# Kernel tuning notes

Measured on AMD Instinct MI355X. Metric: run time of the kernel, lower is better.

## Reference

```python
import jax, jax.numpy as jnp
import numpy as np

E = 2048
H = 16
D = E // H  # head_dim = 128


def setup_inputs() -> dict:
    key = jax.random.key(0)
    ks = jax.random.split(key, 8)
    s = 0.02
    x = jax.random.normal(ks[0], (2, 2048, E), dtype=jnp.float32)
    Wq = jax.random.normal(ks[1], (E, E), dtype=jnp.float32) * s
    Wk = jax.random.normal(ks[2], (E, E), dtype=jnp.float32) * s
    Wv = jax.random.normal(ks[3], (E, E), dtype=jnp.float32) * s
    W1 = jax.random.normal(ks[4], (2 * E, E), dtype=jnp.float32) * s
    b1 = jax.random.normal(ks[5], (2 * E,), dtype=jnp.float32) * s
    W2 = jax.random.normal(ks[6], (E, 2 * E), dtype=jnp.float32) * s
    b2 = jax.random.normal(ks[7], (E,), dtype=jnp.float32) * s
    return {"x": x, "Wq": Wq, "Wk": Wk, "Wv": Wv, "W1": W1, "b1": b1, "W2": W2, "b2": b2}


def reference(x, Wq, Wk, Wv, W1, b1, W2, b2):
    B, S, _ = x.shape
    # QKV projections (torch Linear: x @ W.T), reshape to (B,S,H,D)
    q = (x @ Wq.T).reshape(B, S, H, D)
    k = (x @ Wk.T).reshape(B, S, H, D)
    v = (x @ Wv.T).reshape(B, S, H, D)
    # scores: (B,H,S,S)
    score = jnp.einsum('bqhd,bkhd->bhqk', q, k)
    # causal mask added BEFORE scaling (as in original; -inf unaffected by scale)
    causal = jnp.tril(jnp.ones((S, S), dtype=bool))
    score = jnp.where(causal, score, -jnp.inf)
    score = score / jnp.sqrt(jnp.float32(D))
    attn = jax.nn.softmax(score, axis=-1)
    o = jnp.einsum('bhqk,bkhd->bqhd', attn, v).reshape(B, S, E)
    # FFN with hidden = 2*E, no residual connections in this block
    h = jax.nn.gelu(o @ W1.T + b1)
    return h @ W2.T + b2
```

## Files before the change

### kernel.cpp

```cpp
#include <hip/hip_runtime.h>
#include <cmath>


typedef _Float16 half8 __attribute__((ext_vector_type(8)));
typedef _Float16 half4v __attribute__((ext_vector_type(4)));
typedef float float4v __attribute__((ext_vector_type(4)));

__device__ inline void load_lds16(const _Float16* g, _Float16* l) {
  __builtin_amdgcn_global_load_lds(
      (const __attribute__((address_space(1))) void*)g,
      (__attribute__((address_space(3))) void*)l, 16, 0, 0);
}

__global__ void cvt_kernel(const float* __restrict__ s0, const float* __restrict__ s1,
                           const float* __restrict__ s2, const float* __restrict__ s3,
                           _Float16* d0, _Float16* d1, _Float16* d2, _Float16* d3,
                           int n0, int n1, int n2, int n3, float sc1) {
  const float* s;
  _Float16* d;
  int n;
  float sc = 1.0f;
  switch (blockIdx.y) {
    case 0: s = s0; d = d0; n = n0; break;
    case 1: s = s1; d = d1; n = n1; sc = sc1; break;
    case 2: s = s2; d = d2; n = n2; break;
    default: s = s3; d = d3; n = n3; break;
  }
  const int step = gridDim.x * 256 * 4;
  for (int i = (blockIdx.x * 256 + threadIdx.x) * 4; i < n; i += step) {
    float4v v = *(const float4v*)&s[i];
    half4v h;
#pragma unroll
    for (int e = 0; e < 4; e++) h[e] = (_Float16)(v[e] * sc);
    *(half4v*)&d[i] = h;
  }
}

__device__ __forceinline__ void gemm8_core(
    const _Float16* __restrict__ A, const _Float16* __restrict__ B, int Kloop,
    int Kstride, int bm, int bn, _Float16* lds, float4v acc[8][4]) {
  const int tid = threadIdx.x;
  const int w = tid >> 6, lane = tid & 63;
  const int l16 = lane & 15, quad = lane >> 4;
  const int srow = w * 16 + (lane >> 2);
  const int clocal = ((lane & 3) * 8) ^ ((lane & 32) ? 16 : 0);
  int rdh = (l16 << 5) + (quad << 3);
  rdh ^= (l16 & 8) << 1;

  const _Float16* pA0 = A + (size_t)(bm + srow) * Kstride + clocal;
  const _Float16* pA1 = A + (size_t)(bm + 128 + srow) * Kstride + clocal;
  const _Float16* pB0 = B + (size_t)(bn + srow) * Kstride + clocal;
  const _Float16* pB1 = B + (size_t)(bn + 128 + srow) * Kstride + clocal;

  _Float16* const dA0 = lds + w * 1024;
  _Float16* const dA1 = lds + 8192 + w * 1024;
  _Float16* const dB0 = lds + 16384 + w * 1024;
  _Float16* const dB1 = lds + 24576 + w * 1024;

  const int aH = w >> 2, bH = (w >> 1) & 1, bRB = (w & 1) * 4;
  const _Float16* const rA0 = lds + aH * 8192;
  const _Float16* const rB0 = lds + 16384 + bH * 8192;
  const _Float16* const rA1 = rA0 + 32768;
  const _Float16* const rB1 = rB0 + 32768;

  const int NT = Kloop >> 6;

#define STG(p, d, kt)                     \
  do {                                    \
    const _Float16* _s = (p) + (kt) * 64; \
    load_lds16(_s, (d));                  \
    load_lds16(_s + 32, (d) + 512);       \
  } while (0)
#define BARRIER() asm volatile("s_barrier" ::: "memory")
#define WAIT_LGKM()                                  \
  asm volatile("s_waitcnt lgkmcnt(0)" ::: "memory"); \
  __builtin_amdgcn_sched_barrier(0);
#define RD_A(base, RB0)                                                       \
  _Pragma("unroll") for (int rb = 0; rb < 4; rb++)                            \
  _Pragma("unroll") for (int ks = 0; ks < 2; ks++)                            \
      af[rb][ks] = *(const half8*)&(base)[((((RB0) + rb) * 2 + ks) << 9) + rdh];
#define RD_B(base, J0)                                                        \
  _Pragma("unroll") for (int j = 0; j < 2; j++)                               \
  _Pragma("unroll") for (int ks = 0; ks < 2; ks++)                            \
      bf[(J0) + j][ks] =                                                      \
          *(const half8*)&(base)[(((bRB + (J0) + j) * 2 + ks) << 9) + rdh];
#define MFMA_Q(RB0, J0)                                                       \
  __builtin_amdgcn_s_setprio(1);                                              \
  _Pragma("unroll") for (int rb = 0; rb < 4; rb++)                            \
  _Pragma("unroll") for (int j = 0; j < 2; j++)                               \
  _Pragma("unroll") for (int ks = 0; ks < 2; ks++)                            \
      acc[(RB0) + rb][(J0) + j] = __builtin_amdgcn_mfma_f32_16x16x32_f16(     \
          af[rb][ks], bf[(J0) + j][ks], acc[(RB0) + rb][(J0) + j], 0, 0, 0);  \
  __builtin_amdgcn_s_setprio(0);                                              \
  BARRIER();

  STG(pB0, dB0, 0); STG(pB1, dB1, 0); STG(pA0, dA0, 0); STG(pA1, dA1, 0);
  STG(pB0, dB0 + 32768, 1); STG(pB1, dB1 + 32768, 1);
  asm volatile("s_waitcnt vmcnt(4)" ::: "memory");
  BARRIER();

  half8 af[4][2], bf[4][2];

  for (int t = 0; t < NT; t += 2) {
    const bool last = (t + 2 >= NT);
    RD_A(rA0, 0) RD_B(rB0, 0)
    STG(pA0, dA0 + 32768, t + 1);
    BARRIER(); WAIT_LGKM()
    MFMA_Q(0, 0)
    RD_B(rB0, 2)
    STG(pA1, dA1 + 32768, t + 1);
    BARRIER(); WAIT_LGKM()
    MFMA_Q(0, 2)
    RD_A(rA0, 4)
    if (!last) STG(pB0, dB0, t + 2);
    BARRIER(); WAIT_LGKM()
    MFMA_Q(4, 0)
    if (!last) {
      STG(pA0, dA0, t + 2);
      asm volatile("s_waitcnt vmcnt(4)" ::: "memory");
    } else {
      asm volatile("s_waitcnt vmcnt(0)" ::: "memory");
    }
    BARRIER();
    MFMA_Q(4, 2)
    RD_A(rA1, 0) RD_B(rB1, 0)
    if (!last) STG(pA1, dA1, t + 2);
    BARRIER(); WAIT_LGKM()
    MFMA_Q(0, 0)
    RD_B(rB1, 2)
    if (!last) STG(pB1, dB1, t + 2);
    BARRIER(); WAIT_LGKM()
    MFMA_Q(0, 2)
    RD_A(rA1, 4)
    if (!last) STG(pB0, dB0 + 32768, t + 3);
    BARRIER(); WAIT_LGKM()
    MFMA_Q(4, 0)
    if (!last) {
      STG(pB1, dB1 + 32768, t + 3);
      asm volatile("s_waitcnt vmcnt(4)" ::: "memory");
    }
    BARRIER();
    MFMA_Q(4, 2)
  }
#undef STG
#undef BARRIER
#undef WAIT_LGKM
#undef RD_A
#undef RD_B
#undef MFMA_Q
}

__global__ __launch_bounds__(512, 2) void gemm_qkv(
    const _Float16* __restrict__ xh, const _Float16* __restrict__ Wq,
    const _Float16* __restrict__ Wk, const _Float16* __restrict__ Wv,
    _Float16* __restrict__ Qh, _Float16* __restrict__ Kh,
    _Float16* __restrict__ Vt) {
  __shared__ __align__(16) _Float16 lds[67584];
  const int z = blockIdx.z;
  const _Float16* B = (z == 0) ? Wq : (z == 1 ? Wk : Wv);
  const int bm = blockIdx.y * 256, bn = blockIdx.x * 256;
  float4v acc[8][4] = {};
  gemm8_core(xh, B, 2048, 2048, bm, bn, lds, acc);

  const int tid = threadIdx.x;
  const int w = tid >> 6, lane = tid & 63;
  const int l16 = lane & 15, quad = lane >> 4;
  const int wm = (w >> 2) * 128, wn = (w & 3) * 64;
  if (z == 2) {
    _Float16* Tr = lds;
    __syncthreads();
#pragma unroll
    for (int j = 0; j < 4; j++) {
      const int cl = wn + j * 16 + l16;
#pragma unroll
      for (int rb = 0; rb < 8; rb++) {
        const int ml = wm + rb * 16 + quad * 4;
#pragma unroll
        for (int reg = 0; reg < 4; reg++)
          Tr[cl * 264 + ml + reg] = (_Float16)acc[rb][j][reg];
      }
    }
    __syncthreads();
    const int cl = tid >> 1;
    const int ml = (tid & 1) * 128;
    const int mg = bm + ml;
    _Float16* dst = Vt + ((size_t)(mg >> 11) << 22) +
                    ((size_t)(bn + cl) << 11) + (mg & 2047);
#pragma unroll
    for (int i = 0; i < 16; i++)
      *(half8*)(dst + i * 8) = *(const half8*)&Tr[cl * 264 + ml + i * 8];
  } else {
    _Float16* outRM = z ? Kh : Qh;
#pragma unroll
    for (int j = 0; j < 4; j++) {
      const int col = bn + wn + j * 16 + l16;
#pragma unroll
      for (int rb = 0; rb < 8; rb++) {
        const int rbase = bm + wm + rb * 16 + quad * 4;
#pragma unroll
        for (int reg = 0; reg < 4; reg++)
          outRM[(size_t)(rbase + reg) * 2048 + col] = (_Float16)acc[rb][j][reg];
      }
    }
  }
}

__global__ __launch_bounds__(512, 2) void gemm_ffn1(
    const _Float16* __restrict__ A, const _Float16* __restrict__ B,
    const float* __restrict__ bias, _Float16* __restrict__ out, int N, int K) {
  __shared__ __align__(16) _Float16 lds[65536];
  const int bm = blockIdx.y * 256, bn = blockIdx.x * 256;
  float4v acc[8][4] = {};
  gemm8_core(A, B, K, K, bm, bn, lds, acc);

  const int tid = threadIdx.x;
  const int w = tid >> 6, lane = tid & 63;
  const int l16 = lane & 15, quad = lane >> 4;
  const int wm = (w >> 2) * 128, wn = (w & 3) * 64;
#pragma unroll
  for (int j = 0; j < 4; j++) {
    const int col = bn + wn + j * 16 + l16;
    const float bv = bias[col];
#pragma unroll
    for (int rb = 0; rb < 8; rb++) {
      const int rbase = bm + wm + rb * 16 + quad * 4;
#pragma unroll
      for (int reg = 0; reg < 4; reg++) {
        const int m = rbase + reg;
        const float x = acc[rb][j][reg] + bv;
        const float inner = 0.7978845608028654f * (x + 0.044715f * x * x * x);
        out[(size_t)m * N + col] = (_Float16)(0.5f * x * (1.0f + tanhf(inner)));
      }
    }
  }
}

__global__ __launch_bounds__(512, 2) void gemm_ffn2_part(
    const _Float16* __restrict__ A, const _Float16* __restrict__ B,
    float* __restrict__ p0, float* __restrict__ p1) {
  __shared__ __align__(16) _Float16 lds[65536];
  const int bm = blockIdx.y * 256, bn = blockIdx.x * 256;
  const int k0 = blockIdx.z * 2048;
  float* out = blockIdx.z ? p1 : p0;
  float4v acc[8][4] = {};
  gemm8_core(A + k0, B + k0, 2048, 4096, bm, bn, lds, acc);

  const int tid = threadIdx.x;
  const int w = tid >> 6, lane = tid & 63;
  const int l16 = lane & 15, quad = lane >> 4;
  const int wm = (w >> 2) * 128, wn = (w & 3) * 64;
#pragma unroll
  for (int j = 0; j < 4; j++) {
    const int col = bn + wn + j * 16 + l16;
#pragma unroll
    for (int rb = 0; rb < 8; rb++) {
      const int rbase = bm + wm + rb * 16 + quad * 4;
#pragma unroll
      for (int reg = 0; reg < 4; reg++)
        out[(size_t)(rbase + reg) * 2048 + col] = acc[rb][j][reg];
    }
  }
}

__global__ void reduce_add(float* __restrict__ out, const float* __restrict__ p0,
                           const float* __restrict__ b2, int n) {
  const int step = gridDim.x * 256 * 4;
  for (int i = (blockIdx.x * 256 + threadIdx.x) * 4; i < n; i += step) {
    float4v a = *(const float4v*)&out[i];
    float4v b = *(const float4v*)&p0[i];
    float4v bb = *(const float4v*)&b2[i & 2047];
    float4v r;
#pragma unroll
    for (int e = 0; e < 4; e++) r[e] = a[e] + b[e] + bb[e];
    *(float4v*)&out[i] = r;
  }
}

__global__ __launch_bounds__(256, 2) void attn_mfma(
    const _Float16* __restrict__ Qh, const _Float16* __restrict__ Kh,
    const _Float16* __restrict__ Vt, _Float16* __restrict__ Oh) {
  __shared__ __align__(16) _Float16 Ksh[64][136];
  __shared__ __align__(16) _Float16 Vsh[128][72];
  __shared__ __align__(16) _Float16 Psh[4][32][72];

  const int b = blockIdx.z;
  int qt = blockIdx.x;
  if (b) qt = gridDim.x - 1 - qt;
  const int h = blockIdx.y;
  const int tid = threadIdx.x;
  const int wave = tid >> 6, lane = tid & 63;
  const int l16 = lane & 15, quad = lane >> 4;
  const int q0 = qt * 128;
  const int wq0 = q0 + wave * 32;

  half8 qf[2][4];
#pragma unroll
  for (int rb = 0; rb < 2; rb++)
#pragma unroll
    for (int kc = 0; kc < 4; kc++)
      qf[rb][kc] = *(const half8*)(Qh +
          (size_t)(b * 2048 + wq0 + rb * 16 + l16) * 2048 + h * 128 +
          kc * 32 + quad * 8);

  half8 ones;
#pragma unroll
  for (int e = 0; e < 8; e++) ones[e] = (_Float16)1.0f;

  const int kkey = tid >> 2, kd = (tid & 3) * 32;
  const int vd = tid >> 1, vkey = (tid & 1) * 32;

  half8 kpre[4], vpre[4];
  {
    const _Float16* p = Kh + (size_t)(b * 2048 + kkey) * 2048 + h * 128 + kd;
#pragma unroll
    for (int i = 0; i < 4; i++) kpre[i] = *(const half8*)(p + i * 8);
    const _Float16* pv = Vt + ((size_t)b << 22) + (size_t)(h * 128 + vd) * 2048 + vkey;
#pragma unroll
    for (int i = 0; i < 4; i++) vpre[i] = *(const half8*)(pv + i * 8);
  }

  float4v o[2][9] = {};
  float4v mrow[2];
#pragma unroll
  for (int rb = 0; rb < 2; rb++)
#pragma unroll
    for (int e = 0; e < 4; e++) mrow[rb][e] = -INFINITY;

  const int nkb = qt * 2 + 2;
  for (int kb = 0; kb < nkb; kb++) {
    const int k0 = kb * 64;
    __syncthreads();
#pragma unroll
    for (int i = 0; i < 4; i++) *(half8*)&Ksh[kkey][kd + i * 8] = kpre[i];
#pragma unroll
    for (int i = 0; i < 4; i++) *(half8*)&Vsh[vd][vkey + i * 8] = vpre[i];
    __syncthreads();

    if (kb + 1 < nkb) {
      const int k1 = k0 + 64;
      const _Float16* p = Kh + (size_t)(b * 2048 + k1 + kkey) * 2048 + h * 128 + kd;
#pragma unroll
      for (int i = 0; i < 4; i++) kpre[i] = *(const half8*)(p + i * 8);
      const _Float16* pv = Vt + ((size_t)b << 22) + (size_t)(h * 128 + vd) * 2048 + k1 + vkey;
#pragma unroll
      for (int i = 0; i < 4; i++) vpre[i] = *(const half8*)(pv + i * 8);
    }

    if (k0 <= wq0 + 31) {
      float4v s[2][4] = {};
#pragma unroll
      for (int kc = 0; kc < 4; kc++) {
#pragma unroll
        for (int cb = 0; cb < 4; cb++) {
          half8 kf = *(const half8*)&Ksh[cb * 16 + l16][kc * 32 + quad * 8];
#pragma unroll
          for (int rb = 0; rb < 2; rb++)
            s[rb][cb] = __builtin_amdgcn_mfma_f32_16x16x32_f16(qf[rb][kc], kf, s[rb][cb], 0, 0, 0);
        }
      }
      if (k0 + 63 > wq0) {
#pragma unroll
        for (int cb = 0; cb < 4; cb++)
#pragma unroll
          for (int rb = 0; rb < 2; rb++)
#pragma unroll
            for (int reg = 0; reg < 4; reg++) {
              const int key = k0 + cb * 16 + l16;
              const int row = wq0 + rb * 16 + quad * 4 + reg;
              if (key > row) s[rb][cb][reg] = -INFINITY;
            }
      }
#pragma unroll
      for (int rb = 0; rb < 2; rb++) {
        float4v mt;
#pragma unroll
        for (int e = 0; e < 4; e++)
          mt[e] = fmaxf(fmaxf(s[rb][0][e], s[rb][1][e]),
                        fmaxf(s[rb][2][e], s[rb][3][e]));
#pragma unroll
        for (int msk = 1; msk <= 8; msk <<= 1)
#pragma unroll
          for (int e = 0; e < 4; e++) mt[e] = fmaxf(mt[e], __shfl_xor(mt[e], msk, 64));
        int need = 0;
#pragma unroll
        for (int e = 0; e < 4; e++) need |= (mt[e] > mrow[rb][e] + 8.0f) ? 1 : 0;
        if (__any(need)) {
          float4v al;
#pragma unroll
          for (int e = 0; e < 4; e++) {
            const float mn = fmaxf(mrow[rb][e], mt[e]);
            al[e] = exp2f(mrow[rb][e] - mn);
            mrow[rb][e] = mn;
          }
#pragma unroll
          for (int cd = 0; cd < 9; cd++)
#pragma unroll
            for (int e = 0; e < 4; e++) o[rb][cd][e] *= al[e];
        }
#pragma unroll
        for (int cb = 0; cb < 4; cb++) {
#pragma unroll
          for (int e = 0; e < 4; e++) s[rb][cb][e] = exp2f(s[rb][cb][e] - mrow[rb][e]);
#pragma unroll
          for (int e = 0; e < 4; e++)
            Psh[wave][rb * 16 + quad * 4 + e][cb * 16 + l16] = (_Float16)s[rb][cb][e];
        }
      }
      half8 pf[2][2];
#pragma unroll
      for (int rb = 0; rb < 2; rb++)
#pragma unroll
        for (int kc = 0; kc < 2; kc++)
          pf[rb][kc] = *(const half8*)&Psh[wave][rb * 16 + l16][kc * 32 + quad * 8];
#pragma unroll
      for (int cd = 0; cd < 8; cd++) {
#pragma unroll
        for (int kc = 0; kc < 2; kc++) {
          half8 vf = *(const half8*)&Vsh[cd * 16 + l16][kc * 32 + quad * 8];
#pragma unroll
          for (int rb = 0; rb < 2; rb++)
            o[rb][cd] = __builtin_amdgcn_mfma_f32_16x16x32_f16(pf[rb][kc], vf, o[rb][cd], 0, 0, 0);
        }
      }
#pragma unroll
      for (int kc = 0; kc < 2; kc++)
#pragma unroll
        for (int rb = 0; rb < 2; rb++)
          o[rb][8] = __builtin_amdgcn_mfma_f32_16x16x32_f16(pf[rb][kc], ones, o[rb][8], 0, 0, 0);
    }
  }

#pragma unroll
  for (int rb = 0; rb < 2; rb++) {
    float4v inv;
#pragma unroll
    for (int e = 0; e < 4; e++) inv[e] = 1.0f / o[rb][8][e];
#pragma unroll
    for (int cd = 0; cd < 8; cd++)
#pragma unroll
      for (int reg = 0; reg < 4; reg++)
        Oh[(size_t)(b * 2048 + wq0 + rb * 16 + quad * 4 + reg) * 2048 +
           h * 128 + cd * 16 + l16] = (_Float16)(o[rb][cd][reg] * inv[reg]);
  }
}

extern "C" void kernel_launch(void* const* d_in, const int* in_sizes, int n_in,
                              void* d_out, int out_size, void* d_ws,
                              size_t ws_size, hipStream_t stream) {
  const float* x = (const float*)d_in[0];
  const float* Wq = (const float*)d_in[1];
  const float* Wk = (const float*)d_in[2];
  const float* Wv = (const float*)d_in[3];
  const float* W1 = (const float*)d_in[4];
  const float* b1 = (const float*)d_in[5];
  const float* W2 = (const float*)d_in[6];
  const float* b2 = (const float*)d_in[7];
  float* out = (float*)d_out;

  const int ME = 8388608;
  const int EE = 4194304;

  _Float16* ws = (_Float16*)d_ws;
  _Float16* xh  = ws;
  _Float16* Wqh = xh + ME;
  _Float16* Wkh = Wqh + EE;
  _Float16* Wvh = Wkh + EE;
  _Float16* Qh  = Wvh + EE;
  _Float16* Kh  = Qh + ME;
  _Float16* Vt  = Kh + ME;
  _Float16* Oh  = xh;
  _Float16* W1h = Wqh;
  _Float16* W2h = Vt;
  _Float16* Hid = Qh;
  float*    P0  = (float*)ws;

  const float qscale = 1.4426950408889634f * 0.08838834764831845f;

  cvt_kernel<<<dim3(1024, 4), 256, 0, stream>>>(x, Wq, Wk, Wv, xh, Wqh, Wkh, Wvh,
                                                ME, EE, EE, EE, qscale);
  gemm_qkv<<<dim3(8, 16, 3), 512, 0, stream>>>(xh, Wqh, Wkh, Wvh, Qh, Kh, Vt);
  attn_mfma<<<dim3(16, 16, 2), 256, 0, stream>>>(Qh, Kh, Vt, Oh);
  cvt_kernel<<<dim3(1024, 2), 256, 0, stream>>>(W1, W2, nullptr, nullptr,
                                                W1h, W2h, nullptr, nullptr,
                                                ME, ME, 0, 0, 1.0f);
  gemm_ffn1<<<dim3(16, 16), 512, 0, stream>>>(Oh, W1h, b1, Hid, 4096, 2048);
  gemm_ffn2_part<<<dim3(8, 16, 2), 512, 0, stream>>>(Hid, W2h, P0, out);
  reduce_add<<<dim3(2048), 256, 0, stream>>>(out, P0, b2, ME);
}
```

Before: 546.9 us.

## Stage GEMM and attention epilogues through LDS for vectorized row-major stores

Replaces scattered 2-byte per-element global stores in the QKV, FFN1 and attention output epilogues with a two-pass transpose through XOR-swizzled shared memory, followed by coalesced 16-byte stores. FFN1's tanh-GELU is rewritten as x*sigmoid(2*inner) using exp2f, which is cheaper than tanhf. In attention, the cross-lane max shuffle now runs only when a rescale is actually needed, skipping that reduction on most tiles. The extra barriers and LDS round trips in the epilogues are the cost.

```diff
diff --git a/kernel.cpp b/kernel.cpp
--- a/kernel.cpp
+++ b/kernel.cpp
@@ -150,6 +150,29 @@
 #undef MFMA_Q
 }
 
+#define EPILOGUE_RM(outp, N, VALEXPR)                                         \
+  {                                                                           \
+    _Float16(*Tr)[264] = (_Float16(*)[264])lds;                               \
+    _Pragma("unroll 1") for (int hp = 0; hp < 2; hp++) {                      \
+      __syncthreads();                                                        \
+      if ((w >> 2) == hp) {                                                   \
+        _Pragma("unroll") for (int j = 0; j < 4; j++)                         \
+        _Pragma("unroll") for (int rb = 0; rb < 8; rb++)                      \
+        _Pragma("unroll") for (int reg = 0; reg < 4; reg++) {                 \
+          const int rr = rb * 16 + quad * 4 + reg;                            \
+          Tr[rr][(wn + j * 16 + l16) ^ ((rr & 7) << 3)] =                     \
+              (_Float16)(VALEXPR);                                            \
+        }                                                                     \
+      }                                                                       \
+      __syncthreads();                                                        \
+      const int r = tid >> 2, cc = (tid & 3) * 64;                            \
+      const int xr = (r & 7) << 3;                                            \
+      _Float16* dst = (outp) + (size_t)(bm + hp * 128 + r) * (N) + bn + cc;   \
+      _Pragma("unroll") for (int i = 0; i < 8; i++)                           \
+          *(half8*)(dst + i * 8) = *(const half8*)&Tr[r][(cc + i * 8) ^ xr];  \
+    }                                                                         \
+  }
+
 __global__ __launch_bounds__(512, 2) void gemm_qkv(
     const _Float16* __restrict__ xh, const _Float16* __restrict__ Wq,
     const _Float16* __restrict__ Wk, const _Float16* __restrict__ Wv,
@@ -191,17 +214,7 @@
       *(half8*)(dst + i * 8) = *(const half8*)&Tr[cl * 264 + ml + i * 8];
   } else {
     _Float16* outRM = z ? Kh : Qh;
-#pragma unroll
-    for (int j = 0; j < 4; j++) {
-      const int col = bn + wn + j * 16 + l16;
-#pragma unroll
-      for (int rb = 0; rb < 8; rb++) {
-        const int rbase = bm + wm + rb * 16 + quad * 4;
-#pragma unroll
-        for (int reg = 0; reg < 4; reg++)
-          outRM[(size_t)(rbase + reg) * 2048 + col] = (_Float16)acc[rb][j][reg];
-      }
-    }
+    EPILOGUE_RM(outRM, 2048, acc[rb][j][reg])
   }
 }
 
@@ -216,23 +229,21 @@
   const int tid = threadIdx.x;
   const int w = tid >> 6, lane = tid & 63;
   const int l16 = lane & 15, quad = lane >> 4;
-  const int wm = (w >> 2) * 128, wn = (w & 3) * 64;
+  const int wn = (w & 3) * 64;
 #pragma unroll
   for (int j = 0; j < 4; j++) {
-    const int col = bn + wn + j * 16 + l16;
-    const float bv = bias[col];
-#pragma unroll
-    for (int rb = 0; rb < 8; rb++) {
-      const int rbase = bm + wm + rb * 16 + quad * 4;
+    const float bv = bias[bn + wn + j * 16 + l16];
+#pragma unroll
+    for (int rb = 0; rb < 8; rb++)
 #pragma unroll
       for (int reg = 0; reg < 4; reg++) {
-        const int m = rbase + reg;
         const float x = acc[rb][j][reg] + bv;
-        const float inner = 0.7978845608028654f * (x + 0.044715f * x * x * x);
-        out[(size_t)m * N + col] = (_Float16)(0.5f * x * (1.0f + tanhf(inner)));
+        const float t = x + 0.044715f * x * x * x;
+        const float e = exp2f(-2.302208198f * t);
+        acc[rb][j][reg] = x / (1.0f + e);
       }
-    }
-  }
+  }
+  EPILOGUE_RM(out, N, acc[rb][j][reg])
 }
 
 __global__ __launch_bounds__(512, 2) void gemm_ffn2_part(
@@ -377,14 +388,14 @@
         for (int e = 0; e < 4; e++)
           mt[e] = fmaxf(fmaxf(s[rb][0][e], s[rb][1][e]),
                         fmaxf(s[rb][2][e], s[rb][3][e]));
-#pragma unroll
-        for (int msk = 1; msk <= 8; msk <<= 1)
-#pragma unroll
-          for (int e = 0; e < 4; e++) mt[e] = fmaxf(mt[e], __shfl_xor(mt[e], msk, 64));
         int need = 0;
 #pragma unroll
         for (int e = 0; e < 4; e++) need |= (mt[e] > mrow[rb][e] + 8.0f) ? 1 : 0;
         if (__any(need)) {
+#pragma unroll
+          for (int msk = 1; msk <= 8; msk <<= 1)
+#pragma unroll
+            for (int e = 0; e < 4; e++) mt[e] = fmaxf(mt[e], __shfl_xor(mt[e], msk, 64));
           float4v al;
 #pragma unroll
           for (int e = 0; e < 4; e++) {
@@ -430,17 +441,32 @@
     }
   }
 
-#pragma unroll
-  for (int rb = 0; rb < 2; rb++) {
-    float4v inv;
-#pragma unroll
-    for (int e = 0; e < 4; e++) inv[e] = 1.0f / o[rb][8][e];
-#pragma unroll
-    for (int cd = 0; cd < 8; cd++)
-#pragma unroll
-      for (int reg = 0; reg < 4; reg++)
-        Oh[(size_t)(b * 2048 + wq0 + rb * 16 + quad * 4 + reg) * 2048 +
-           h * 128 + cd * 16 + l16] = (_Float16)(o[rb][cd][reg] * inv[reg]);
+  float4v inv[2];
+#pragma unroll
+  for (int rb = 0; rb < 2; rb++)
+#pragma unroll
+    for (int e = 0; e < 4; e++) inv[rb][e] = 1.0f / o[rb][8][e];
+
+#pragma unroll 1
+  for (int p = 0; p < 2; p++) {
+    __syncthreads();
+    if ((wave >> 1) == p) {
+      _Float16* slab = &Ksh[(wave & 1) * 32][0];
+#pragma unroll
+      for (int rb = 0; rb < 2; rb++)
+#pragma unroll
+        for (int cd = 0; cd < 8; cd++)
+#pragma unroll
+          for (int reg = 0; reg < 4; reg++)
+            slab[(rb * 16 + quad * 4 + reg) * 136 + cd * 16 + l16] =
+                (_Float16)(o[rb][cd][reg] * inv[rb][reg]);
+    }
+    __syncthreads();
+    const int r = tid >> 2, c = (tid & 3) * 8;
+    _Float16* dst = Oh + (size_t)(b * 2048 + q0 + p * 64 + r) * 2048 + h * 128 + c;
+#pragma unroll
+    for (int i = 0; i < 4; i++)
+      *(half8*)(dst + i * 32) = *(const half8*)&Ksh[r][c + i * 32];
   }
 }
 
```

Result: slower. 566.5 us (+3.6%).

## Enlarge attention tiles to 256 queries and 128-key blocks, stage output via LDS

Applied to the files above, without the earlier changes.

The attention kernel moves to 512-thread blocks, each covering 256 query rows, and processes 128 keys per iteration. This halves the number of K/V tile loads and barriers per query row. The cross-lane max reduction now runs only when a rescale is needed, and the output is staged through LDS so global writes are coalesced 16-byte stores. GELU in FFN1 is rewritten from tanh to an equivalent exp2-based sigmoid form. In exchange the kernel uses much more LDS, which limits it to one block per CU, and it drops the reversed-tile ordering that balanced causal work across batches.

```diff
diff --git a/kernel.cpp b/kernel.cpp
--- a/kernel.cpp
+++ b/kernel.cpp
@@ -228,8 +228,9 @@
       for (int reg = 0; reg < 4; reg++) {
         const int m = rbase + reg;
         const float x = acc[rb][j][reg] + bv;
-        const float inner = 0.7978845608028654f * (x + 0.044715f * x * x * x);
-        out[(size_t)m * N + col] = (_Float16)(0.5f * x * (1.0f + tanhf(inner)));
+        const float t = x + 0.044715f * x * x * x;
+        const float e = exp2f(-2.302208198f * t);
+        out[(size_t)m * N + col] = (_Float16)(x / (1.0f + e));
       }
     }
   }
@@ -276,21 +277,20 @@
   }
 }
 
-__global__ __launch_bounds__(256, 2) void attn_mfma(
+__global__ __launch_bounds__(512, 2) void attn_mfma(
     const _Float16* __restrict__ Qh, const _Float16* __restrict__ Kh,
     const _Float16* __restrict__ Vt, _Float16* __restrict__ Oh) {
-  __shared__ __align__(16) _Float16 Ksh[64][136];
-  __shared__ __align__(16) _Float16 Vsh[128][72];
-  __shared__ __align__(16) _Float16 Psh[4][32][72];
+  __shared__ __align__(16) _Float16 Ksh[128][136];
+  __shared__ __align__(16) _Float16 Vsh[128][136];
+  __shared__ __align__(16) _Float16 Psh[8][32][136];
 
   const int b = blockIdx.z;
-  int qt = blockIdx.x;
-  if (b) qt = gridDim.x - 1 - qt;
+  const int qt = blockIdx.x;
   const int h = blockIdx.y;
   const int tid = threadIdx.x;
   const int wave = tid >> 6, lane = tid & 63;
   const int l16 = lane & 15, quad = lane >> 4;
-  const int q0 = qt * 128;
+  const int q0 = qt * 256;
   const int wq0 = q0 + wave * 32;
 
   half8 qf[2][4];
@@ -307,7 +307,7 @@
   for (int e = 0; e < 8; e++) ones[e] = (_Float16)1.0f;
 
   const int kkey = tid >> 2, kd = (tid & 3) * 32;
-  const int vd = tid >> 1, vkey = (tid & 1) * 32;
+  const int vd = tid >> 2, vkey = (tid & 3) * 32;
 
   half8 kpre[4], vpre[4];
   {
@@ -328,7 +328,7 @@
 
   const int nkb = qt * 2 + 2;
   for (int kb = 0; kb < nkb; kb++) {
-    const int k0 = kb * 64;
+    const int k0 = kb * 128;
     __syncthreads();
 #pragma unroll
     for (int i = 0; i < 4; i++) *(half8*)&Ksh[kkey][kd + i * 8] = kpre[i];
@@ -337,7 +337,7 @@
     __syncthreads();
 
     if (kb + 1 < nkb) {
-      const int k1 = k0 + 64;
+      const int k1 = k0 + 128;
       const _Float16* p = Kh + (size_t)(b * 2048 + k1 + kkey) * 2048 + h * 128 + kd;
 #pragma unroll
       for (int i = 0; i < 4; i++) kpre[i] = *(const half8*)(p + i * 8);
@@ -347,20 +347,20 @@
     }
 
     if (k0 <= wq0 + 31) {
-      float4v s[2][4] = {};
+      float4v s[2][8] = {};
 #pragma unroll
       for (int kc = 0; kc < 4; kc++) {
 #pragma unroll
-        for (int cb = 0; cb < 4; cb++) {
+        for (int cb = 0; cb < 8; cb++) {
           half8 kf = *(const half8*)&Ksh[cb * 16 + l16][kc * 32 + quad * 8];
 #pragma unroll
           for (int rb = 0; rb < 2; rb++)
             s[rb][cb] = __builtin_amdgcn_mfma_f32_16x16x32_f16(qf[rb][kc], kf, s[rb][cb], 0, 0, 0);
         }
       }
-      if (k0 + 63 > wq0) {
-#pragma unroll
-        for (int cb = 0; cb < 4; cb++)
+      if (k0 + 127 > wq0) {
+#pragma unroll
+        for (int cb = 0; cb < 8; cb++)
 #pragma unroll
           for (int rb = 0; rb < 2; rb++)
 #pragma unroll
@@ -374,17 +374,21 @@
       for (int rb = 0; rb < 2; rb++) {
         float4v mt;
 #pragma unroll
-        for (int e = 0; e < 4; e++)
-          mt[e] = fmaxf(fmaxf(s[rb][0][e], s[rb][1][e]),
-                        fmaxf(s[rb][2][e], s[rb][3][e]));
-#pragma unroll
-        for (int msk = 1; msk <= 8; msk <<= 1)
-#pragma unroll
-          for (int e = 0; e < 4; e++) mt[e] = fmaxf(mt[e], __shfl_xor(mt[e], msk, 64));
+        for (int e = 0; e < 4; e++) {
+          float m01 = fmaxf(s[rb][0][e], s[rb][1][e]);
+          float m23 = fmaxf(s[rb][2][e], s[rb][3][e]);
+          float m45 = fmaxf(s[rb][4][e], s[rb][5][e]);
+          float m67 = fmaxf(s[rb][6][e], s[rb][7][e]);
+          mt[e] = fmaxf(fmaxf(m01, m23), fmaxf(m45, m67));
+        }
         int need = 0;
 #pragma unroll
         for (int e = 0; e < 4; e++) need |= (mt[e] > mrow[rb][e] + 8.0f) ? 1 : 0;
         if (__any(need)) {
+#pragma unroll
+          for (int msk = 1; msk <= 8; msk <<= 1)
+#pragma unroll
+            for (int e = 0; e < 4; e++) mt[e] = fmaxf(mt[e], __shfl_xor(mt[e], msk, 64));
           float4v al;
 #pragma unroll
           for (int e = 0; e < 4; e++) {
@@ -398,7 +402,7 @@
             for (int e = 0; e < 4; e++) o[rb][cd][e] *= al[e];
         }
 #pragma unroll
-        for (int cb = 0; cb < 4; cb++) {
+        for (int cb = 0; cb < 8; cb++) {
 #pragma unroll
           for (int e = 0; e < 4; e++) s[rb][cb][e] = exp2f(s[rb][cb][e] - mrow[rb][e]);
 #pragma unroll
@@ -406,16 +410,16 @@
             Psh[wave][rb * 16 + quad * 4 + e][cb * 16 + l16] = (_Float16)s[rb][cb][e];
         }
       }
-      half8 pf[2][2];
+      half8 pf[2][4];
 #pragma unroll
       for (int rb = 0; rb < 2; rb++)
 #pragma unroll
-        for (int kc = 0; kc < 2; kc++)
+        for (int kc = 0; kc < 4; kc++)
           pf[rb][kc] = *(const half8*)&Psh[wave][rb * 16 + l16][kc * 32 + quad * 8];
 #pragma unroll
       for (int cd = 0; cd < 8; cd++) {
 #pragma unroll
-        for (int kc = 0; kc < 2; kc++) {
+        for (int kc = 0; kc < 4; kc++) {
           half8 vf = *(const half8*)&Vsh[cd * 16 + l16][kc * 32 + quad * 8];
 #pragma unroll
           for (int rb = 0; rb < 2; rb++)
@@ -423,24 +427,39 @@
         }
       }
 #pragma unroll
-      for (int kc = 0; kc < 2; kc++)
+      for (int kc = 0; kc < 4; kc++)
 #pragma unroll
         for (int rb = 0; rb < 2; rb++)
           o[rb][8] = __builtin_amdgcn_mfma_f32_16x16x32_f16(pf[rb][kc], ones, o[rb][8], 0, 0, 0);
     }
   }
 
-#pragma unroll
-  for (int rb = 0; rb < 2; rb++) {
-    float4v inv;
-#pragma unroll
-    for (int e = 0; e < 4; e++) inv[e] = 1.0f / o[rb][8][e];
-#pragma unroll
-    for (int cd = 0; cd < 8; cd++)
-#pragma unroll
-      for (int reg = 0; reg < 4; reg++)
-        Oh[(size_t)(b * 2048 + wq0 + rb * 16 + quad * 4 + reg) * 2048 +
-           h * 128 + cd * 16 + l16] = (_Float16)(o[rb][cd][reg] * inv[reg]);
+  float4v inv[2];
+#pragma unroll
+  for (int rb = 0; rb < 2; rb++)
+#pragma unroll
+    for (int e = 0; e < 4; e++) inv[rb][e] = 1.0f / o[rb][8][e];
+
+#pragma unroll 1
+  for (int p = 0; p < 2; p++) {
+    __syncthreads();
+    if ((wave >> 2) == p) {
+      _Float16* slab = &Ksh[(wave & 3) * 32][0];
+#pragma unroll
+      for (int rb = 0; rb < 2; rb++)
+#pragma unroll
+        for (int cd = 0; cd < 8; cd++)
+#pragma unroll
+          for (int reg = 0; reg < 4; reg++)
+            slab[(rb * 16 + quad * 4 + reg) * 136 + cd * 16 + l16] =
+                (_Float16)(o[rb][cd][reg] * inv[rb][reg]);
+    }
+    __syncthreads();
+    const int r = tid >> 2, c = (tid & 3) * 32;
+    _Float16* dst = Oh + (size_t)(b * 2048 + q0 + p * 128 + r) * 2048 + h * 128 + c;
+#pragma unroll
+    for (int i = 0; i < 4; i++)
+      *(half8*)(dst + i * 8) = *(const half8*)&Ksh[r][c + i * 8];
   }
 }
 
@@ -479,7 +498,7 @@
   cvt_kernel<<<dim3(1024, 4), 256, 0, stream>>>(x, Wq, Wk, Wv, xh, Wqh, Wkh, Wvh,
                                                 ME, EE, EE, EE, qscale);
   gemm_qkv<<<dim3(8, 16, 3), 512, 0, stream>>>(xh, Wqh, Wkh, Wvh, Qh, Kh, Vt);
-  attn_mfma<<<dim3(16, 16, 2), 256, 0, stream>>>(Qh, Kh, Vt, Oh);
+  attn_mfma<<<dim3(8, 16, 2), 512, 0, stream>>>(Qh, Kh, Vt, Oh);
   cvt_kernel<<<dim3(1024, 2), 256, 0, stream>>>(W1, W2, nullptr, nullptr,
                                                 W1h, W2h, nullptr, nullptr,
                                                 ME, ME, 0, 0, 1.0f);
```

Measured after the change: 574.4 us. +5.0%, slower.

## Swizzle attention LDS tiles, stage output stores, cheaper GELU, higher occupancy

Applied to the files above, without the earlier changes.

Replaces the padded K/V/P shared-memory tiles in the attention kernel with XOR-swizzled unpadded layouts. This shrinks LDS use so the launch bound can request 3 blocks per SM instead of 2. The output tile is now staged through LDS so global writes are coalesced 16-byte stores. The row-max shuffle reduction is moved inside the rare rescale branch, and the FFN1 GELU tanh is rewritten as an exp2-based sigmoid form. Risks include register pressure from the higher occupancy target and a slightly stale per-lane max estimate, which is bounded by the +8 threshold.

```diff
diff --git a/kernel.cpp b/kernel.cpp
--- a/kernel.cpp
+++ b/kernel.cpp
@@ -228,8 +228,9 @@
       for (int reg = 0; reg < 4; reg++) {
         const int m = rbase + reg;
         const float x = acc[rb][j][reg] + bv;
-        const float inner = 0.7978845608028654f * (x + 0.044715f * x * x * x);
-        out[(size_t)m * N + col] = (_Float16)(0.5f * x * (1.0f + tanhf(inner)));
+        const float t = x + 0.044715f * x * x * x;
+        const float e = exp2f(-2.302208198f * t);
+        out[(size_t)m * N + col] = (_Float16)(x / (1.0f + e));
       }
     }
   }
@@ -276,12 +277,12 @@
   }
 }
 
-__global__ __launch_bounds__(256, 2) void attn_mfma(
+__global__ __launch_bounds__(256, 3) void attn_mfma(
     const _Float16* __restrict__ Qh, const _Float16* __restrict__ Kh,
     const _Float16* __restrict__ Vt, _Float16* __restrict__ Oh) {
-  __shared__ __align__(16) _Float16 Ksh[64][136];
-  __shared__ __align__(16) _Float16 Vsh[128][72];
-  __shared__ __align__(16) _Float16 Psh[4][32][72];
+  __shared__ __align__(16) _Float16 Ksh[8192];
+  __shared__ __align__(16) _Float16 Vsh[8192];
+  __shared__ __align__(16) _Float16 Psh[4][2048];
 
   const int b = blockIdx.z;
   int qt = blockIdx.x;
@@ -292,6 +293,7 @@
   const int l16 = lane & 15, quad = lane >> 4;
   const int q0 = qt * 128;
   const int wq0 = q0 + wave * 32;
+  const int rxor = (l16 & 7) << 3;
 
   half8 qf[2][4];
 #pragma unroll
@@ -308,6 +310,8 @@
 
   const int kkey = tid >> 2, kd = (tid & 3) * 32;
   const int vd = tid >> 1, vkey = (tid & 1) * 32;
+  const int kswz = (kkey & 7) << 3;
+  const int vswz = (vd & 7) << 3;
 
   half8 kpre[4], vpre[4];
   {
@@ -331,9 +335,11 @@
     const int k0 = kb * 64;
     __syncthreads();
 #pragma unroll
-    for (int i = 0; i < 4; i++) *(half8*)&Ksh[kkey][kd + i * 8] = kpre[i];
-#pragma unroll
-    for (int i = 0; i < 4; i++) *(half8*)&Vsh[vd][vkey + i * 8] = vpre[i];
+    for (int i = 0; i < 4; i++)
+      *(half8*)&Ksh[kkey * 128 + ((kd + i * 8) ^ kswz)] = kpre[i];
+#pragma unroll
+    for (int i = 0; i < 4; i++)
+      *(half8*)&Vsh[vd * 64 + ((vkey + i * 8) ^ vswz)] = vpre[i];
     __syncthreads();
 
     if (kb + 1 < nkb) {
@@ -352,7 +358,8 @@
       for (int kc = 0; kc < 4; kc++) {
 #pragma unroll
         for (int cb = 0; cb < 4; cb++) {
-          half8 kf = *(const half8*)&Ksh[cb * 16 + l16][kc * 32 + quad * 8];
+          half8 kf = *(const half8*)&Ksh[(cb * 16 + l16) * 128 +
+                                         ((kc * 32 + quad * 8) ^ rxor)];
 #pragma unroll
           for (int rb = 0; rb < 2; rb++)
             s[rb][cb] = __builtin_amdgcn_mfma_f32_16x16x32_f16(qf[rb][kc], kf, s[rb][cb], 0, 0, 0);
@@ -377,14 +384,14 @@
         for (int e = 0; e < 4; e++)
           mt[e] = fmaxf(fmaxf(s[rb][0][e], s[rb][1][e]),
                         fmaxf(s[rb][2][e], s[rb][3][e]));
-#pragma unroll
-        for (int msk = 1; msk <= 8; msk <<= 1)
-#pragma unroll
-          for (int e = 0; e < 4; e++) mt[e] = fmaxf(mt[e], __shfl_xor(mt[e], msk, 64));
         int need = 0;
 #pragma unroll
         for (int e = 0; e < 4; e++) need |= (mt[e] > mrow[rb][e] + 8.0f) ? 1 : 0;
         if (__any(need)) {
+#pragma unroll
+          for (int msk = 1; msk <= 8; msk <<= 1)
+#pragma unroll
+            for (int e = 0; e < 4; e++) mt[e] = fmaxf(mt[e], __shfl_xor(mt[e], msk, 64));
           float4v al;
 #pragma unroll
           for (int e = 0; e < 4; e++) {
@@ -402,8 +409,11 @@
 #pragma unroll
           for (int e = 0; e < 4; e++) s[rb][cb][e] = exp2f(s[rb][cb][e] - mrow[rb][e]);
 #pragma unroll
-          for (int e = 0; e < 4; e++)
-            Psh[wave][rb * 16 + quad * 4 + e][cb * 16 + l16] = (_Float16)s[rb][cb][e];
+          for (int e = 0; e < 4; e++) {
+            const int pr = rb * 16 + quad * 4 + e;
+            Psh[wave][pr * 64 + ((cb * 16 + l16) ^ ((pr & 7) << 3))] =
+                (_Float16)s[rb][cb][e];
+          }
         }
       }
       half8 pf[2][2];
@@ -411,12 +421,14 @@
       for (int rb = 0; rb < 2; rb++)
 #pragma unroll
         for (int kc = 0; kc < 2; kc++)
-          pf[rb][kc] = *(const half8*)&Psh[wave][rb * 16 + l16][kc * 32 + quad * 8];
+          pf[rb][kc] = *(const half8*)&Psh[wave][(rb * 16 + l16) * 64 +
+                                                 ((kc * 32 + quad * 8) ^ rxor)];
 #pragma unroll
       for (int cd = 0; cd < 8; cd++) {
 #pragma unroll
         for (int kc = 0; kc < 2; kc++) {
-          half8 vf = *(const half8*)&Vsh[cd * 16 + l16][kc * 32 + quad * 8];
+          half8 vf = *(const half8*)&Vsh[(cd * 16 + l16) * 64 +
+                                         ((kc * 32 + quad * 8) ^ rxor)];
 #pragma unroll
           for (int rb = 0; rb < 2; rb++)
             o[rb][cd] = __builtin_amdgcn_mfma_f32_16x16x32_f16(pf[rb][kc], vf, o[rb][cd], 0, 0, 0);
@@ -430,17 +442,35 @@
     }
   }
 
-#pragma unroll
-  for (int rb = 0; rb < 2; rb++) {
-    float4v inv;
-#pragma unroll
-    for (int e = 0; e < 4; e++) inv[e] = 1.0f / o[rb][8][e];
-#pragma unroll
-    for (int cd = 0; cd < 8; cd++)
-#pragma unroll
-      for (int reg = 0; reg < 4; reg++)
-        Oh[(size_t)(b * 2048 + wq0 + rb * 16 + quad * 4 + reg) * 2048 +
-           h * 128 + cd * 16 + l16] = (_Float16)(o[rb][cd][reg] * inv[reg]);
+  float4v inv[2];
+#pragma unroll
+  for (int rb = 0; rb < 2; rb++)
+#pragma unroll
+    for (int e = 0; e < 4; e++) inv[rb][e] = 1.0f / o[rb][8][e];
+
+#pragma unroll 1
+  for (int p = 0; p < 2; p++) {
+    __syncthreads();
+    if ((wave >> 1) == p) {
+      _Float16* slab = &Ksh[(wave & 1) * 32 * 128];
+#pragma unroll
+      for (int rb = 0; rb < 2; rb++)
+#pragma unroll
+        for (int cd = 0; cd < 8; cd++)
+#pragma unroll
+          for (int reg = 0; reg < 4; reg++) {
+            const int rr = rb * 16 + quad * 4 + reg;
+            slab[rr * 128 + ((cd * 16 + l16) ^ ((rr & 7) << 3))] =
+                (_Float16)(o[rb][cd][reg] * inv[rb][reg]);
+          }
+    }
+    __syncthreads();
+    const int r = tid >> 2, c = (tid & 3) * 8;
+    const int oxor = (r & 7) << 3;
+    _Float16* dst = Oh + (size_t)(b * 2048 + q0 + p * 64 + r) * 2048 + h * 128 + c;
+#pragma unroll
+    for (int i = 0; i < 4; i++)
+      *(half8*)(dst + i * 32) = *(const half8*)&Ksh[r * 128 + ((c + i * 32) ^ oxor)];
   }
 }
 
```

Result: slower. 781.2 us (+42.9%).
